# Optimization experiments

Hardware: AMD Instinct MI355X
Metric: run time of the kernel (lower is better)

Reference implementation:

```python
import jax, jax.numpy as jnp
import numpy as np

TOPK = 2


def setup_inputs() -> dict:
    key = jax.random.key(0)
    k1, k2 = jax.random.split(key)
    B, N, D, E, C = 4, 2048, 2048, 8, 512
    token_inputs = jax.random.normal(k1, (B, N, D), dtype=jnp.float32)
    # bottleneck_in.weight.t() stacked over experts: [E, D, C]; scaled like a real init
    bottleneck_weights = jax.random.normal(k2, (E, D, C), dtype=jnp.float32) * 0.02
    return {
        "token_inputs": token_inputs,
        "bottleneck_weights": bottleneck_weights,
        "expert_capacity": 640,
    }


def _routing(router_probs, expert_capacity, topk):
    # router_probs: [B, N, E]
    B, N, E = router_probs.shape
    _, expert_indices = jax.lax.top_k(router_probs, topk)      # [B, N, topk]
    idx = jnp.transpose(expert_indices, (0, 2, 1)).reshape(B, topk * N)
    expert_mask = jax.nn.one_hot(idx, E, dtype=jnp.int32)       # [B, topk*N, E]
    token_priority = jnp.cumsum(expert_mask, axis=1) * expert_mask - 1
    token_priority = token_priority.reshape(B, topk, N, E)
    token_priority = jnp.transpose(token_priority, (0, 2, 1, 3))  # [B, N, topk, E]
    token_priority = jnp.max(token_priority, axis=2)              # [B, N, E]
    # one-hot over capacity; negative (-1) and >= capacity priorities map to all-zero rows
    cap_range = jnp.arange(expert_capacity, dtype=jnp.int32)
    dispatch = (token_priority[..., None] == cap_range).astype(jnp.float32)  # [B,N,E,C]
    combine = router_probs[..., None] * dispatch                            # [B,N,E,C]
    return dispatch, combine


def reference(token_inputs, bottleneck_weights, expert_capacity):
    # activation_cache: [B, N, E, Cb]
    activation_cache = jnp.einsum("bnd,edc->bnec", token_inputs, bottleneck_weights)
    router_logits = jnp.sqrt(jnp.sum(activation_cache * activation_cache, axis=-1))  # [B,N,E]
    router_probs = jax.nn.softmax(router_logits, axis=-1)
    dispatch, combine = _routing(router_probs, expert_capacity, TOPK)
    return jnp.stack([dispatch, combine], axis=0)  # [2, B, N, E, capacity]
```

## Files before the change

kernel.cpp:

```cpp
#include <hip/hip_runtime.h>
#include <math.h>

constexpr int Bb = 4, Nn = 2048, Dd = 2048, Ee = 8, Cbn = 512;
constexpr int Mm = Bb * Nn;

typedef _Float16 half8 __attribute__((ext_vector_type(8)));
typedef float floatx16 __attribute__((ext_vector_type(16)));

#define GLL16(g, l)                                                     \
  __builtin_amdgcn_global_load_lds(                                     \
      (const __attribute__((address_space(1))) void*)(g),               \
      (__attribute__((address_space(3))) void*)(l), 16, 0, 0)

#define MFMA_F16(a, b, c) __builtin_amdgcn_mfma_f32_32x32x16_f16(a, b, c, 0, 0, 0)


__global__ __launch_bounds__(256) void prep_kernel(const float* __restrict__ W,
                                                   _Float16* __restrict__ WT,
                                                   const float* __restrict__ X,
                                                   _Float16* __restrict__ XT) {
  __shared__ _Float16 thi[64][72];
  __shared__ _Float16 tlo[64][72];
  const int bid = blockIdx.x;
  if (bid < 2048) {
    const int kt = bid & 31;
    const int ct = (bid >> 5) & 7;
    const int e = bid >> 8;
    const int tx = threadIdx.x & 15, ty = threadIdx.x >> 4;
    const float* src = W + ((size_t)(e * 2048 + kt * 64)) * 512 + ct * 64;
#pragma unroll
    for (int p = 0; p < 4; ++p) {
      int kk = ty + p * 16;
      float4 v = *(const float4*)(src + (size_t)kk * 512 + tx * 4);
      _Float16 hh;
      hh = (_Float16)v.x; thi[tx * 4 + 0][kk] = hh; tlo[tx * 4 + 0][kk] = (_Float16)(v.x - (float)hh);
      hh = (_Float16)v.y; thi[tx * 4 + 1][kk] = hh; tlo[tx * 4 + 1][kk] = (_Float16)(v.y - (float)hh);
      hh = (_Float16)v.z; thi[tx * 4 + 2][kk] = hh; tlo[tx * 4 + 2][kk] = (_Float16)(v.z - (float)hh);
      hh = (_Float16)v.w; thi[tx * 4 + 3][kk] = hh; tlo[tx * 4 + 3][kk] = (_Float16)(v.w - (float)hh);
    }
    __syncthreads();
    const int nt = e * 4 + (ct >> 1);
#pragma unroll
    for (int p = 0; p < 2; ++p) {
      int unit = threadIdx.x + p * 256;
      int ch = unit >> 6;
      int cc = unit & 63;
      int kt16 = kt * 4 + (ch >> 1);
      int chunk = ch & 1;
      int row = (ct & 1) * 64 + cc;
      _Float16* dst = WT + ((size_t)(nt * 128 + kt16)) * 4096 + chunk * 1024 + row * 8;
      *(half8*)dst = *(const half8*)(&thi[cc][ch * 8]);
      *(half8*)(dst + 2048) = *(const half8*)(&tlo[cc][ch * 8]);
    }
  } else {
    const int id = bid - 2048;
    const int mt = id & 63;
    const int kb = id >> 6;
    const int tid = threadIdx.x;
#pragma unroll
    for (int p = 0; p < 2; ++p) {
      const int u = tid + p * 256;
      const int c4 = u & 3;
      const int row = u >> 2;
      const float* src = X + ((size_t)(mt * 128 + row)) * 2048 + kb * 32 + c4 * 8;
      float4 a = *(const float4*)src;
      float4 b = *(const float4*)(src + 4);
      float f[8] = {a.x, a.y, a.z, a.w, b.x, b.y, b.z, b.w};
      half8 hi, lo;
#pragma unroll
      for (int j = 0; j < 8; ++j) {
        _Float16 hh = (_Float16)f[j];
        hi[j] = hh;
        lo[j] = (_Float16)(f[j] - (float)hh);
      }
      const int kt16 = kb * 2 + (c4 >> 1);
      const int chunk = c4 & 1;
      _Float16* dst = XT + ((size_t)(mt * 128 + kt16)) * 4096 + chunk * 1024 + row * 8;
      *(half8*)dst = hi;
      *(half8*)(dst + 2048) = lo;
    }
  }
}

__global__ __launch_bounds__(512) void gemm_mfma(const _Float16* __restrict__ XT,
                                                 const _Float16* __restrict__ WT,
                                                 float* __restrict__ partial) {
  const int bid = blockIdx.x;
  const int swz = (bid & 7) * 64 + (bid >> 3);
  const int bM = swz >> 4;
  const int bN = swz & 15;

  const int tid = threadIdx.x;
  const int w = tid >> 6, l = tid & 63;
  const int wm = w >> 2, wn = w & 3;
  const int h = l >> 5, l31 = l & 31;

  __shared__ __align__(16) char lds[131072];

  const char* XTb = (const char*)XT;
  const char* WTb = (const char*)WT;
  const char* srcA[4];
  const char* srcB[4];
  int ldsAo[4], ldsBo[4];
#pragma unroll
  for (int q = 0; q < 4; ++q) {
    const int c = q * 8 + w;
    const int ht = c >> 4, k16 = (c >> 3) & 1, u = c & 7;
    srcA[q] = XTb + (size_t)(bM * 2 + ht) * 1048576 + k16 * 8192 + u * 1024 + l * 16;
    srcB[q] = WTb + (size_t)(bN * 2 + ht) * 1048576 + k16 * 8192 + u * 1024 + l * 16;
    ldsAo[q] = c * 1024;
    ldsBo[q] = 32768 + c * 1024;
  }

  int aoff[2][4][2], boff[2][2][2];
#pragma unroll
  for (int k16 = 0; k16 < 2; ++k16) {
#pragma unroll
    for (int mf = 0; mf < 4; ++mf)
#pragma unroll
      for (int hl = 0; hl < 2; ++hl)
        aoff[k16][mf][hl] = wm * 16384 + k16 * 8192 + hl * 4096 + h * 2048 +
                            (mf * 32 + l31) * 16;
#pragma unroll
    for (int nf = 0; nf < 2; ++nf)
#pragma unroll
      for (int hl = 0; hl < 2; ++hl)
        boff[k16][nf][hl] = 32768 + (wn >> 1) * 16384 + k16 * 8192 + hl * 4096 + h * 2048 +
                            ((wn & 1) * 64 + nf * 32 + l31) * 16;
  }

  floatx16 acc[4][2] = {};

  auto stage = [&](int t) {
    const size_t ko = (size_t)t * 16384;
    char* base = lds + (t & 1) * 65536;
#pragma unroll
    for (int q = 0; q < 4; ++q) {
      GLL16(srcA[q] + ko, base + ldsAo[q]);
      GLL16(srcB[q] + ko, base + ldsBo[q]);
    }
  };
  auto compute = [&](int t) {
    const char* Lb = lds + (t & 1) * 65536;
#pragma unroll
    for (int k16 = 0; k16 < 2; ++k16) {
      half8 ah[4], al[4], bh[2], bl[2];
#pragma unroll
      for (int mf = 0; mf < 4; ++mf) {
        ah[mf] = *(const half8*)(Lb + aoff[k16][mf][0]);
        al[mf] = *(const half8*)(Lb + aoff[k16][mf][1]);
      }
#pragma unroll
      for (int nf = 0; nf < 2; ++nf) {
        bh[nf] = *(const half8*)(Lb + boff[k16][nf][0]);
        bl[nf] = *(const half8*)(Lb + boff[k16][nf][1]);
      }
      __builtin_amdgcn_s_setprio(1);
#pragma unroll
      for (int mf = 0; mf < 4; ++mf)
#pragma unroll
        for (int nf = 0; nf < 2; ++nf) {
          acc[mf][nf] = MFMA_F16(ah[mf], bh[nf], acc[mf][nf]);
          acc[mf][nf] = MFMA_F16(ah[mf], bl[nf], acc[mf][nf]);
          acc[mf][nf] = MFMA_F16(al[mf], bh[nf], acc[mf][nf]);
        }
      __builtin_amdgcn_s_setprio(0);
    }
  };

  stage(0);
  asm volatile("s_waitcnt vmcnt(0)" ::: "memory");
  __builtin_amdgcn_s_barrier();

  for (int kt = 0; kt < 63; ++kt) {
    stage(kt + 1);
    compute(kt);
    asm volatile("s_waitcnt vmcnt(0)" ::: "memory");
    __builtin_amdgcn_s_barrier();
  }
  compute(63);

  const int slice = bN * 4 + wn;
  float out0 = 0.f, out1 = 0.f;
#pragma unroll
  for (int j = 0; j < 2; ++j) {
    float mv = 0.f;
#pragma unroll
    for (int ii = 0; ii < 2; ++ii) {
      const floatx16& c0 = acc[j * 2 + ii][0];
      const floatx16& c1 = acc[j * 2 + ii][1];
#pragma unroll
      for (int reg = 0; reg < 16; ++reg) {
        float v = c0[reg] * c0[reg] + c1[reg] * c1[reg];
#pragma unroll
        for (int m = 1; m <= 16; m <<= 1) v += __shfl_xor(v, m, 64);
        if (l31 == ii * 16 + reg) mv = v;
      }
    }
    if (j == 0) out0 = mv; else out1 = mv;
  }
  {
    const int reg = l & 15;
    const int ii = l31 >> 4;
    const int rowin = (reg & 3) + 8 * (reg >> 2) + 4 * h;
    const int tok = bM * 256 + wm * 128 + ii * 32 + rowin;
    partial[(size_t)tok * 64 + slice] = out0;
    partial[(size_t)(tok + 64) * 64 + slice] = out1;
  }
}

__global__ __launch_bounds__(1024) void route_scan(const float* __restrict__ partial,
                                                   int* __restrict__ idx1,
                                                   int* __restrict__ idx2,
                                                   float* __restrict__ p1,
                                                   float* __restrict__ p2,
                                                   int* __restrict__ prios) {
  const int b = blockIdx.x;
  const int tid = threadIdx.x;
  __shared__ unsigned char e1s[2048], e2s[2048];
  __shared__ int cnts[1024][9];

#pragma unroll
  for (int r = 0; r < 2; ++r) {
    const int n = tid * 2 + r;
    const int t = b * 2048 + n;
    const float4* pr = (const float4*)(partial + (size_t)t * 64);
    float l[Ee];
    float mx = -1e30f;
#pragma unroll
    for (int e = 0; e < Ee; ++e) {
      float4 s0 = pr[e * 2], s1 = pr[e * 2 + 1];
      float s = s0.x + s0.y + s0.z + s0.w + s1.x + s1.y + s1.z + s1.w;
      l[e] = sqrtf(s);
      mx = fmaxf(mx, l[e]);
    }
    float p[Ee];
    float s = 0.f;
#pragma unroll
    for (int e = 0; e < Ee; ++e) {
      p[e] = expf(l[e] - mx);
      s += p[e];
    }
    float inv = 1.f / s;
    int i1 = 0;
    float b1 = l[0];
#pragma unroll
    for (int e = 1; e < Ee; ++e)
      if (l[e] > b1) { b1 = l[e]; i1 = e; }
    int i2 = -1;
    float b2 = -1e30f;
#pragma unroll
    for (int e = 0; e < Ee; ++e)
      if (e != i1 && l[e] > b2) { b2 = l[e]; i2 = e; }
    idx1[t] = i1;
    idx2[t] = i2;
    p1[t] = p[i1] * inv;
    p2[t] = p[i2] * inv;
    e1s[n] = (unsigned char)i1;
    e2s[n] = (unsigned char)i2;
  }
  __syncthreads();

  int cnt[Ee] = {0, 0, 0, 0, 0, 0, 0, 0};
  int eloc[4];
#pragma unroll
  for (int i = 0; i < 4; ++i) {
    const int p = tid * 4 + i;
    const int e = (p >> 11) ? (int)e2s[p & 2047] : (int)e1s[p & 2047];
    eloc[i] = e;
    cnt[e]++;
  }
#pragma unroll
  for (int e = 0; e < Ee; ++e) cnts[tid][e] = cnt[e];
  __syncthreads();

  const int wv = tid >> 6, ln = tid & 63;
  if (wv < 8) {
    int loc[16];
    int s = 0;
#pragma unroll
    for (int i = 0; i < 16; ++i) {
      loc[i] = cnts[ln * 16 + i][wv];
      s += loc[i];
    }
    int x = s;
#pragma unroll
    for (int off = 1; off < 64; off <<= 1) {
      int y = __shfl_up(x, off, 64);
      if (ln >= off) x += y;
    }
    int run = x - s;
#pragma unroll
    for (int i = 0; i < 16; ++i) {
      int tmp = loc[i];
      cnts[ln * 16 + i][wv] = run;
      run += tmp;
    }
  }
  __syncthreads();

  int base[Ee];
#pragma unroll
  for (int e = 0; e < Ee; ++e) base[e] = cnts[tid][e];
#pragma unroll
  for (int i = 0; i < 4; ++i) {
    prios[b * 4096 + tid * 4 + i] = base[eloc[i]]++;
  }
}

__global__ __launch_bounds__(256) void zscatter_kernel(const int* __restrict__ idx1,
                                                       const int* __restrict__ idx2,
                                                       const float* __restrict__ p1,
                                                       const float* __restrict__ p2,
                                                       const int* __restrict__ prios,
                                                       float* __restrict__ out, int cap) {
  const int t = blockIdx.x;
  const int ec = Ee * cap;
  float4* o1 = (float4*)(out + (size_t)t * ec);
  float4* o2 = (float4*)(out + (size_t)(Mm + t) * ec);
  const float4 z = make_float4(0.f, 0.f, 0.f, 0.f);
  const int n4 = ec / 4;
  for (int i = threadIdx.x; i < n4; i += 256) {
    o1[i] = z;
    o2[i] = z;
  }
  __syncthreads();
  if (threadIdx.x == 0) {
    const int b = t >> 11;
    const int n = t & (Nn - 1);
    int e = idx1[t];
    int p = prios[b * 2 * Nn + n];
    if (p < cap) {
      out[(size_t)t * ec + e * cap + p] = 1.f;
      out[(size_t)(Mm + t) * ec + e * cap + p] = p1[t];
    }
    e = idx2[t];
    p = prios[b * 2 * Nn + Nn + n];
    if (p < cap) {
      out[(size_t)t * ec + e * cap + p] = 1.f;
      out[(size_t)(Mm + t) * ec + e * cap + p] = p2[t];
    }
  }
}

extern "C" void kernel_launch(void* const* d_in, const int* in_sizes, int n_in,
                              void* d_out, int out_size, void* d_ws, size_t ws_size,
                              hipStream_t stream) {
  const float* X = (const float*)d_in[0];
  const float* W = (const float*)d_in[1];
  float* out = (float*)d_out;
  const int cap = out_size / (2 * Bb * Nn * Ee);

  char* ws = (char*)d_ws;
  _Float16* WT = (_Float16*)ws;
  float* partial = (float*)(ws + 33554432ull);
  int* idx1 = (int*)(ws + 35651584ull);
  int* idx2 = idx1 + Mm;
  float* p1 = (float*)(idx2 + Mm);
  float* p2 = p1 + Mm;
  int* prios = (int*)(p2 + Mm);

  _Float16* XT = (_Float16*)d_out;

  prep_kernel<<<6144, 256, 0, stream>>>(W, WT, X, XT);
  gemm_mfma<<<512, 512, 0, stream>>>(XT, WT, partial);
  route_scan<<<Bb, 1024, 0, stream>>>(partial, idx1, idx2, p1, p2, prios);
  zscatter_kernel<<<Mm, 256, 0, stream>>>(idx1, idx2, p1, p2, prios, out, cap);
}
```

Before: 763.3 us.

## Split K across wave groups in GEMM and fuse one-hot writes into zero fill

```diff
diff --git a/kernel.cpp b/kernel.cpp
--- a/kernel.cpp
+++ b/kernel.cpp
@@ -92,7 +92,7 @@
 
   const int tid = threadIdx.x;
   const int w = tid >> 6, l = tid & 63;
-  const int wm = w >> 2, wn = w & 3;
+  const int qp = w & 3, qm = qp >> 1, qn = qp & 1, ks = w >> 2;
   const int h = l >> 5, l31 = l & 31;
 
   __shared__ __align__(16) char lds[131072];
@@ -112,24 +112,21 @@
     ldsBo[q] = 32768 + c * 1024;
   }
 
-  int aoff[2][4][2], boff[2][2][2];
-#pragma unroll
-  for (int k16 = 0; k16 < 2; ++k16) {
-#pragma unroll
-    for (int mf = 0; mf < 4; ++mf)
-#pragma unroll
-      for (int hl = 0; hl < 2; ++hl)
-        aoff[k16][mf][hl] = wm * 16384 + k16 * 8192 + hl * 4096 + h * 2048 +
-                            (mf * 32 + l31) * 16;
-#pragma unroll
-    for (int nf = 0; nf < 2; ++nf)
-#pragma unroll
-      for (int hl = 0; hl < 2; ++hl)
-        boff[k16][nf][hl] = 32768 + (wn >> 1) * 16384 + k16 * 8192 + hl * 4096 + h * 2048 +
-                            ((wn & 1) * 64 + nf * 32 + l31) * 16;
-  }
-
-  floatx16 acc[4][2] = {};
+  int aoff[4][2], boff[4][2];
+#pragma unroll
+  for (int mf = 0; mf < 4; ++mf)
+#pragma unroll
+    for (int hl = 0; hl < 2; ++hl)
+      aoff[mf][hl] = qm * 16384 + ks * 8192 + hl * 4096 + h * 2048 +
+                     (mf * 32 + l31) * 16;
+#pragma unroll
+  for (int nf = 0; nf < 4; ++nf)
+#pragma unroll
+    for (int hl = 0; hl < 2; ++hl)
+      boff[nf][hl] = 32768 + qn * 16384 + ks * 8192 + hl * 4096 + h * 2048 +
+                     (nf * 32 + l31) * 16;
+
+  floatx16 acc[4][4] = {};
 
   auto stage = [&](int t) {
     const size_t ko = (size_t)t * 16384;
@@ -142,27 +139,29 @@
   };
   auto compute = [&](int t) {
     const char* Lb = lds + (t & 1) * 65536;
-#pragma unroll
-    for (int k16 = 0; k16 < 2; ++k16) {
-      half8 ah[4], al[4], bh[2], bl[2];
-#pragma unroll
-      for (int mf = 0; mf < 4; ++mf) {
-        ah[mf] = *(const half8*)(Lb + aoff[k16][mf][0]);
-        al[mf] = *(const half8*)(Lb + aoff[k16][mf][1]);
-      }
-#pragma unroll
-      for (int nf = 0; nf < 2; ++nf) {
-        bh[nf] = *(const half8*)(Lb + boff[k16][nf][0]);
-        bl[nf] = *(const half8*)(Lb + boff[k16][nf][1]);
+    half8 ah[4], al[4];
+#pragma unroll
+    for (int mf = 0; mf < 4; ++mf) {
+      ah[mf] = *(const half8*)(Lb + aoff[mf][0]);
+      al[mf] = *(const half8*)(Lb + aoff[mf][1]);
+    }
+#pragma unroll
+    for (int hn = 0; hn < 2; ++hn) {
+      half8 bh[2], bl[2];
+#pragma unroll
+      for (int j = 0; j < 2; ++j) {
+        bh[j] = *(const half8*)(Lb + boff[hn * 2 + j][0]);
+        bl[j] = *(const half8*)(Lb + boff[hn * 2 + j][1]);
       }
       __builtin_amdgcn_s_setprio(1);
 #pragma unroll
       for (int mf = 0; mf < 4; ++mf)
 #pragma unroll
-        for (int nf = 0; nf < 2; ++nf) {
-          acc[mf][nf] = MFMA_F16(ah[mf], bh[nf], acc[mf][nf]);
-          acc[mf][nf] = MFMA_F16(ah[mf], bl[nf], acc[mf][nf]);
-          acc[mf][nf] = MFMA_F16(al[mf], bh[nf], acc[mf][nf]);
+        for (int j = 0; j < 2; ++j) {
+          const int nf = hn * 2 + j;
+          acc[mf][nf] = MFMA_F16(ah[mf], bh[j], acc[mf][nf]);
+          acc[mf][nf] = MFMA_F16(ah[mf], bl[j], acc[mf][nf]);
+          acc[mf][nf] = MFMA_F16(al[mf], bh[j], acc[mf][nf]);
         }
       __builtin_amdgcn_s_setprio(0);
     }
@@ -180,32 +179,55 @@
   }
   compute(63);
 
-  const int slice = bN * 4 + wn;
-  float out0 = 0.f, out1 = 0.f;
-#pragma unroll
-  for (int j = 0; j < 2; ++j) {
-    float mv = 0.f;
-#pragma unroll
-    for (int ii = 0; ii < 2; ++ii) {
-      const floatx16& c0 = acc[j * 2 + ii][0];
-      const floatx16& c1 = acc[j * 2 + ii][1];
-#pragma unroll
-      for (int reg = 0; reg < 16; ++reg) {
-        float v = c0[reg] * c0[reg] + c1[reg] * c1[reg];
-#pragma unroll
-        for (int m = 1; m <= 16; m <<= 1) v += __shfl_xor(v, m, 64);
-        if (l31 == ii * 16 + reg) mv = v;
+#pragma unroll
+  for (int mf = 0; mf < 4; ++mf) {
+    if (ks == 1) {
+#pragma unroll
+      for (int nf = 0; nf < 4; ++nf)
+#pragma unroll
+        for (int rg = 0; rg < 4; ++rg) {
+          float4 v = make_float4(acc[mf][nf][rg * 4 + 0], acc[mf][nf][rg * 4 + 1],
+                                 acc[mf][nf][rg * 4 + 2], acc[mf][nf][rg * 4 + 3]);
+          *(float4*)(lds + qp * 16384 + nf * 4096 + rg * 1024 + l * 16) = v;
+        }
+    }
+    __syncthreads();
+    if (ks == 0) {
+#pragma unroll
+      for (int nf = 0; nf < 4; ++nf)
+#pragma unroll
+        for (int rg = 0; rg < 4; ++rg) {
+          float4 v = *(const float4*)(lds + qp * 16384 + nf * 4096 + rg * 1024 + l * 16);
+          acc[mf][nf][rg * 4 + 0] += v.x;
+          acc[mf][nf][rg * 4 + 1] += v.y;
+          acc[mf][nf][rg * 4 + 2] += v.z;
+          acc[mf][nf][rg * 4 + 3] += v.w;
+        }
+    }
+    __syncthreads();
+  }
+
+  if (ks == 0) {
+#pragma unroll
+    for (int mf = 0; mf < 4; ++mf)
+#pragma unroll
+      for (int g = 0; g < 2; ++g) {
+        float mv = 0.f;
+#pragma unroll
+        for (int reg = 0; reg < 16; ++reg) {
+          float v = acc[mf][g * 2][reg] * acc[mf][g * 2][reg] +
+                    acc[mf][g * 2 + 1][reg] * acc[mf][g * 2 + 1][reg];
+#pragma unroll
+          for (int m = 1; m <= 16; m <<= 1) v += __shfl_xor(v, m, 64);
+          if (l31 == reg) mv = v;
+        }
+        if (l31 < 16) {
+          const int rowin = (l31 & 3) + 8 * (l31 >> 2) + 4 * h;
+          const int tok = bM * 256 + qm * 128 + mf * 32 + rowin;
+          const int slice = bN * 4 + qn * 2 + g;
+          partial[(size_t)tok * 64 + slice] = mv;
+        }
       }
-    }
-    if (j == 0) out0 = mv; else out1 = mv;
-  }
-  {
-    const int reg = l & 15;
-    const int ii = l31 >> 4;
-    const int rowin = (reg & 3) + 8 * (reg >> 2) + 4 * h;
-    const int tok = bM * 256 + wm * 128 + ii * 32 + rowin;
-    partial[(size_t)tok * 64 + slice] = out0;
-    partial[(size_t)(tok + 64) * 64 + slice] = out1;
   }
 }
 
@@ -316,30 +338,30 @@
                                                        float* __restrict__ out, int cap) {
   const int t = blockIdx.x;
   const int ec = Ee * cap;
+  const int b = t >> 11;
+  const int n = t & (Nn - 1);
+  const int e1 = idx1[t], e2 = idx2[t];
+  const int q1 = prios[b * 2 * Nn + n];
+  const int q2 = prios[b * 2 * Nn + Nn + n];
+  const float v1 = p1[t], v2 = p2[t];
+  const int d1 = (q1 < cap) ? e1 * cap + q1 : -1;
+  const int d2 = (q2 < cap) ? e2 * cap + q2 : -1;
   float4* o1 = (float4*)(out + (size_t)t * ec);
   float4* o2 = (float4*)(out + (size_t)(Mm + t) * ec);
-  const float4 z = make_float4(0.f, 0.f, 0.f, 0.f);
   const int n4 = ec / 4;
   for (int i = threadIdx.x; i < n4; i += 256) {
-    o1[i] = z;
-    o2[i] = z;
-  }
-  __syncthreads();
-  if (threadIdx.x == 0) {
-    const int b = t >> 11;
-    const int n = t & (Nn - 1);
-    int e = idx1[t];
-    int p = prios[b * 2 * Nn + n];
-    if (p < cap) {
-      out[(size_t)t * ec + e * cap + p] = 1.f;
-      out[(size_t)(Mm + t) * ec + e * cap + p] = p1[t];
-    }
-    e = idx2[t];
-    p = prios[b * 2 * Nn + Nn + n];
-    if (p < cap) {
-      out[(size_t)t * ec + e * cap + p] = 1.f;
-      out[(size_t)(Mm + t) * ec + e * cap + p] = p2[t];
-    }
+    const int base = i * 4;
+    float4 dv, cv;
+    dv.x = (d1 == base + 0 || d2 == base + 0) ? 1.f : 0.f;
+    dv.y = (d1 == base + 1 || d2 == base + 1) ? 1.f : 0.f;
+    dv.z = (d1 == base + 2 || d2 == base + 2) ? 1.f : 0.f;
+    dv.w = (d1 == base + 3 || d2 == base + 3) ? 1.f : 0.f;
+    cv.x = (d1 == base + 0) ? v1 : ((d2 == base + 0) ? v2 : 0.f);
+    cv.y = (d1 == base + 1) ? v1 : ((d2 == base + 1) ? v2 : 0.f);
+    cv.z = (d1 == base + 2) ? v1 : ((d2 == base + 2) ? v2 : 0.f);
+    cv.w = (d1 == base + 3) ? v1 : ((d2 == base + 3) ? v2 : 0.f);
+    o1[i] = dv;
+    o2[i] = cv;
   }
 }
 
```

Result: slower. 1.834 ms (+140.3%).
